# Performance work log

Hardware: AMD Instinct MI355X
Metric: run time of the kernel (lower is better)

The kernel has to match this reference:

```python
import jax, jax.numpy as jnp
import numpy as np
from jax import lax

BETA = 0.95
THRESHOLD = 1.0
B, T, D_IN, D_OUT = 128, 512, 512, 512


def setup_inputs() -> dict:
    key = jax.random.key(0)
    k1, k2, k3 = jax.random.split(key, 3)
    x_seq = jax.random.normal(k1, (B, T, D_IN), dtype=jnp.float32)
    W = jax.random.normal(k2, (D_OUT, D_IN), dtype=jnp.float32) * (1.0 / np.sqrt(D_IN))
    b = jax.random.normal(k3, (D_OUT,), dtype=jnp.float32) * 0.01
    return {"x_seq": x_seq, "W": W, "b": b}


def reference(x_seq, W, b):
    # Batch the linear across all timesteps: [B,T,D_in] @ [D_out,D_in]^T -> [B,T,D_out]
    currents = jnp.einsum('bti,oi->bto', x_seq, W) + b

    def step(mem, cur):  # mem: [B, D_out], cur: [B, D_out]
        mem = BETA * mem + cur
        spk = (mem > THRESHOLD).astype(mem.dtype)
        return mem - spk * THRESHOLD, spk

    mem0 = jnp.zeros((x_seq.shape[0], W.shape[0]), dtype=x_seq.dtype)
    _, spikes_tbd = lax.scan(step, mem0, jnp.swapaxes(currents, 0, 1))  # [T,B,D]
    spikes = jnp.swapaxes(spikes_tbd, 0, 1)  # [B,T,D]
    return spikes, spikes.sum()
```

## Files before the change

kernel.cpp:

```cpp
#include <hip/hip_runtime.h>
#include <hip/hip_bf16.h>

#define M_TOT 65536
#define K_DIM 512
#define N_DIM 512
#define T_STEPS 512
#define BETA 0.95f

#define BM 128
#define BN 128
#define BK 64

typedef __attribute__((ext_vector_type(8))) short bf16x8;
typedef __attribute__((ext_vector_type(8))) unsigned short u16x8;
typedef __attribute__((ext_vector_type(4))) float f32x4;

#define X_ELEMS ((size_t)M_TOT * K_DIM)
#define W_ELEMS ((size_t)N_DIM * K_DIM)
#define WS_NEEDED ((X_ELEMS + W_ELEMS + X_ELEMS) * 2)

static __device__ __forceinline__ unsigned short f2bf(float f) {
    __hip_bfloat16 h = __float2bfloat16(f);
    return __builtin_bit_cast(unsigned short, h);
}
static __device__ __forceinline__ float bf2f(unsigned short u) {
    return __builtin_bit_cast(float, (unsigned int)u << 16);
}

__global__ __launch_bounds__(256) void convert_bf16(
    const float* __restrict__ X, const float* __restrict__ W,
    unsigned short* __restrict__ Xb, unsigned short* __restrict__ Wb,
    float* __restrict__ sum_out)
{
    const size_t gid = (size_t)blockIdx.x * 256 + threadIdx.x;
    if (gid == 0) *sum_out = 0.0f;
    const size_t NXT = X_ELEMS / 8;
    if (gid < NXT) {
        const float4 v0 = *(const float4*)(X + gid * 8);
        const float4 v1 = *(const float4*)(X + gid * 8 + 4);
        u16x8 o;
        o[0] = f2bf(v0.x); o[1] = f2bf(v0.y); o[2] = f2bf(v0.z); o[3] = f2bf(v0.w);
        o[4] = f2bf(v1.x); o[5] = f2bf(v1.y); o[6] = f2bf(v1.z); o[7] = f2bf(v1.w);
        *(u16x8*)(Xb + gid * 8) = o;
    } else {
        const size_t g2 = gid - NXT;
        const float4 v0 = *(const float4*)(W + g2 * 8);
        const float4 v1 = *(const float4*)(W + g2 * 8 + 4);
        u16x8 o;
        o[0] = f2bf(v0.x); o[1] = f2bf(v0.y); o[2] = f2bf(v0.z); o[3] = f2bf(v0.w);
        o[4] = f2bf(v1.x); o[5] = f2bf(v1.y); o[6] = f2bf(v1.z); o[7] = f2bf(v1.w);
        *(u16x8*)(Wb + g2 * 8) = o;
    }
}

__global__ __launch_bounds__(256) void gemm_fast(
    const unsigned short* __restrict__ Xb,
    const unsigned short* __restrict__ Wb,
    const float* __restrict__ bias,
    unsigned short* __restrict__ Cb)
{
    __shared__ alignas(16) unsigned short Xs[2][BM][BK];
    __shared__ alignas(16) unsigned short Ws[2][BN][BK];

    const int lin  = blockIdx.x;
    const int swz  = (lin & 7) * 256 + (lin >> 3);
    const int mtile = swz >> 2;
    const int ntile = swz & 3;

    const int tid  = threadIdx.x;
    const int lane = tid & 63;
    const int wave = tid >> 6;
    const int wr = wave >> 1;
    const int wc = wave & 1;

    const int row0 = mtile * BM;
    const int col0 = ntile * BN;

    f32x4 acc[4][4] = {};

    const int srow = lane >> 3;
    const int scb  = (lane & 7) ^ (srow & 7);
    const unsigned short* xsrc[4];
    const unsigned short* wsrc[4];
    #pragma unroll
    for (int j = 0; j < 4; ++j) {
        const int ra = row0 + wave * 32 + j * 8 + srow;
        const int rb = col0 + wave * 32 + j * 8 + srow;
        xsrc[j] = Xb + (size_t)ra * K_DIM + scb * 8;
        wsrc[j] = Wb + (size_t)rb * K_DIM + scb * 8;
    }

    const int frow = lane & 15;
    const int cblk = lane >> 4;

    #pragma unroll
    for (int j = 0; j < 4; ++j) {
        __builtin_amdgcn_global_load_lds(
            (const __attribute__((address_space(1))) unsigned int*)(const void*)(xsrc[j]),
            (__attribute__((address_space(3))) unsigned int*)(void*)(&Xs[0][wave * 32 + j * 8][0]),
            16, 0, 0);
        __builtin_amdgcn_global_load_lds(
            (const __attribute__((address_space(1))) unsigned int*)(const void*)(wsrc[j]),
            (__attribute__((address_space(3))) unsigned int*)(void*)(&Ws[0][wave * 32 + j * 8][0]),
            16, 0, 0);
    }

    #pragma unroll
    for (int t = 0; t < 8; ++t) {
        const int cur = t & 1;
        __syncthreads();

        if (t < 7) {
            #pragma unroll
            for (int j = 0; j < 4; ++j) {
                __builtin_amdgcn_global_load_lds(
                    (const __attribute__((address_space(1))) unsigned int*)(const void*)(xsrc[j] + (t + 1) * BK),
                    (__attribute__((address_space(3))) unsigned int*)(void*)(&Xs[cur ^ 1][wave * 32 + j * 8][0]),
                    16, 0, 0);
                __builtin_amdgcn_global_load_lds(
                    (const __attribute__((address_space(1))) unsigned int*)(const void*)(wsrc[j] + (t + 1) * BK),
                    (__attribute__((address_space(3))) unsigned int*)(void*)(&Ws[cur ^ 1][wave * 32 + j * 8][0]),
                    16, 0, 0);
            }
        }

        #pragma unroll
        for (int kh = 0; kh < 2; ++kh) {
            bf16x8 afr[4], bfr[4];
            #pragma unroll
            for (int m = 0; m < 4; ++m) {
                int row = wr * 64 + m * 16 + frow;
                int c = (kh * 4 + cblk) ^ (row & 7);
                afr[m] = *(const bf16x8*)(&Xs[cur][row][c * 8]);
            }
            #pragma unroll
            for (int n = 0; n < 4; ++n) {
                int row = wc * 64 + n * 16 + frow;
                int c = (kh * 4 + cblk) ^ (row & 7);
                bfr[n] = *(const bf16x8*)(&Ws[cur][row][c * 8]);
            }
            #pragma unroll
            for (int m = 0; m < 4; ++m)
                #pragma unroll
                for (int n = 0; n < 4; ++n)
                    acc[m][n] = __builtin_amdgcn_mfma_f32_16x16x32_bf16(
                        afr[m], bfr[n], acc[m][n], 0, 0, 0);
        }
    }

    const int crow_base = (lane >> 4) * 4;
    const int ccol = lane & 15;
    #pragma unroll
    for (int n = 0; n < 4; ++n) {
        int col = col0 + wc * 64 + n * 16 + ccol;
        float bv = bias[col];
        #pragma unroll
        for (int m = 0; m < 4; ++m) {
            int rowb = row0 + wr * 64 + m * 16 + crow_base;
            #pragma unroll
            for (int r = 0; r < 4; ++r) {
                Cb[(size_t)(rowb + r) * N_DIM + col] = f2bf(acc[m][n][r] + bv);
            }
        }
    }
}

__global__ __launch_bounds__(256) void lif_scan(
    const unsigned short* __restrict__ Cb,
    float* __restrict__ S,
    float* __restrict__ sum_out)
{
    const int idx = blockIdx.x * 256 + threadIdx.x;
    const size_t base = (size_t)(idx >> 9) * (T_STEPS * N_DIM) + (idx & 511);
    const unsigned short* p = Cb + base;
    float* q = S + base;

    float mem = 0.0f;
    int count = 0;
    float a[32], b[32];

    #pragma unroll
    for (int j = 0; j < 32; ++j)
        a[j] = bf2f(p[(size_t)j * N_DIM]);

    for (int t = 0; t < T_STEPS; t += 64) {
        #pragma unroll
        for (int j = 0; j < 32; ++j)
            b[j] = bf2f(p[(size_t)(t + 32 + j) * N_DIM]);
        #pragma unroll
        for (int j = 0; j < 32; ++j) {
            mem = BETA * mem + a[j];
            float spk = (mem > 1.0f) ? 1.0f : 0.0f;
            mem -= spk;
            __builtin_nontemporal_store(spk, q + (size_t)(t + j) * N_DIM);
            count += (int)spk;
        }
        if (t + 64 < T_STEPS) {
            #pragma unroll
            for (int j = 0; j < 32; ++j)
                a[j] = bf2f(p[(size_t)(t + 64 + j) * N_DIM]);
        }
        #pragma unroll
        for (int j = 0; j < 32; ++j) {
            mem = BETA * mem + b[j];
            float spk = (mem > 1.0f) ? 1.0f : 0.0f;
            mem -= spk;
            __builtin_nontemporal_store(spk, q + (size_t)(t + 32 + j) * N_DIM);
            count += (int)spk;
        }
    }

    #pragma unroll
    for (int off = 32; off > 0; off >>= 1)
        count += __shfl_down(count, off);
    __shared__ int wsum[4];
    if ((threadIdx.x & 63) == 0) wsum[threadIdx.x >> 6] = count;
    __syncthreads();
    if (threadIdx.x == 0) {
        int tot = wsum[0] + wsum[1] + wsum[2] + wsum[3];
        atomicAdd(sum_out, (float)tot);
    }
}

static __device__ __forceinline__ void stage_tiles(
    unsigned short (*__restrict__ Xs)[BK], unsigned short (*__restrict__ Ws)[BK],
    const float4* xr, const float4* wv, int sr0, int skg)
{
    #pragma unroll
    for (int i = 0; i < 8; ++i) {
        int r   = sr0 + i * 16;
        int kgs = skg ^ ((r & 7) << 3);
        ushort4 xb, wb;
        xb.x = f2bf(xr[i].x); xb.y = f2bf(xr[i].y); xb.z = f2bf(xr[i].z); xb.w = f2bf(xr[i].w);
        wb.x = f2bf(wv[i].x); wb.y = f2bf(wv[i].y); wb.z = f2bf(wv[i].z); wb.w = f2bf(wv[i].w);
        *(ushort4*)(&Xs[r][kgs]) = xb;
        *(ushort4*)(&Ws[r][kgs]) = wb;
    }
}

__global__ __launch_bounds__(256, 2) void gemm_slow(
    const float* __restrict__ X, const float* __restrict__ W,
    const float* __restrict__ bias, float* __restrict__ C,
    float* __restrict__ sum_out)
{
    __shared__ unsigned short Xs[2][BM][BK];
    __shared__ unsigned short Ws[2][BN][BK];

    const int lin  = blockIdx.x;
    const int swz  = (lin & 7) * 256 + (lin >> 3);
    const int mtile = swz >> 2;
    const int ntile = swz & 3;

    const int tid  = threadIdx.x;
    const int lane = tid & 63;
    const int wave = tid >> 6;
    const int wr = wave >> 1;
    const int wc = wave & 1;

    if (lin == 0 && tid == 0) *sum_out = 0.0f;

    const int row0 = mtile * BM;
    const int col0 = ntile * BN;

    f32x4 acc[4][4] = {};

    const int sr0 = tid >> 4;
    const int skg = (tid & 15) << 2;
    const float* xbase = X + (size_t)row0 * K_DIM + skg;
    const float* wbase = W + (size_t)col0 * K_DIM + skg;

    float4 xr[8], wv[8];
    #pragma unroll
    for (int i = 0; i < 8; ++i) {
        int r = sr0 + i * 16;
        xr[i] = *(const float4*)(xbase + (size_t)r * K_DIM);
        wv[i] = *(const float4*)(wbase + (size_t)r * K_DIM);
    }
    stage_tiles(Xs[0], Ws[0], xr, wv, sr0, skg);

    const int frow = lane & 15;
    const int cblk = lane >> 4;

    for (int t = 0; t < 8; ++t) {
        __syncthreads();
        if (t < 7) {
            const int k0n = (t + 1) * BK;
            #pragma unroll
            for (int i = 0; i < 8; ++i) {
                int r = sr0 + i * 16;
                xr[i] = *(const float4*)(xbase + (size_t)r * K_DIM + k0n);
                wv[i] = *(const float4*)(wbase + (size_t)r * K_DIM + k0n);
            }
        }
        unsigned short (*Xbuf)[BK] = Xs[t & 1];
        unsigned short (*Wbuf)[BK] = Ws[t & 1];
        #pragma unroll
        for (int kh = 0; kh < 2; ++kh) {
            bf16x8 afr[4], bfr[4];
            #pragma unroll
            for (int m = 0; m < 4; ++m) {
                int row = wr * 64 + m * 16 + frow;
                int c = (kh * 4 + cblk) ^ (row & 7);
                afr[m] = *(const bf16x8*)(&Xbuf[row][c * 8]);
            }
            #pragma unroll
            for (int n = 0; n < 4; ++n) {
                int row = wc * 64 + n * 16 + frow;
                int c = (kh * 4 + cblk) ^ (row & 7);
                bfr[n] = *(const bf16x8*)(&Wbuf[row][c * 8]);
            }
            #pragma unroll
            for (int m = 0; m < 4; ++m)
                #pragma unroll
                for (int n = 0; n < 4; ++n)
                    acc[m][n] = __builtin_amdgcn_mfma_f32_16x16x32_bf16(
                        afr[m], bfr[n], acc[m][n], 0, 0, 0);
        }
        if (t < 7)
            stage_tiles(Xs[(t + 1) & 1], Ws[(t + 1) & 1], xr, wv, sr0, skg);
    }

    const int crow_base = (lane >> 4) * 4;
    const int ccol = lane & 15;
    #pragma unroll
    for (int n = 0; n < 4; ++n) {
        int col = col0 + wc * 64 + n * 16 + ccol;
        float bv = bias[col];
        #pragma unroll
        for (int m = 0; m < 4; ++m) {
            int rowb = row0 + wr * 64 + m * 16 + crow_base;
            #pragma unroll
            for (int r = 0; r < 4; ++r) {
                C[(size_t)(rowb + r) * N_DIM + col] = acc[m][n][r] + bv;
            }
        }
    }
}

__global__ __launch_bounds__(256) void lif_scan_f32(
    float* __restrict__ C, float* __restrict__ sum_out)
{
    const int idx = blockIdx.x * 256 + threadIdx.x;
    float* p = C + (size_t)(idx >> 9) * (T_STEPS * N_DIM) + (idx & 511);
    float mem = 0.0f;
    int count = 0;
    for (int t = 0; t < T_STEPS; t += 8) {
        float cur[8];
        #pragma unroll
        for (int j = 0; j < 8; ++j) cur[j] = p[(size_t)(t + j) * N_DIM];
        #pragma unroll
        for (int j = 0; j < 8; ++j) {
            mem = BETA * mem + cur[j];
            float spk = (mem > 1.0f) ? 1.0f : 0.0f;
            mem -= spk;
            p[(size_t)(t + j) * N_DIM] = spk;
            count += (int)spk;
        }
    }
    #pragma unroll
    for (int off = 32; off > 0; off >>= 1) count += __shfl_down(count, off);
    __shared__ int wsum[4];
    if ((threadIdx.x & 63) == 0) wsum[threadIdx.x >> 6] = count;
    __syncthreads();
    if (threadIdx.x == 0)
        atomicAdd(sum_out, (float)(wsum[0] + wsum[1] + wsum[2] + wsum[3]));
}

extern "C" void kernel_launch(void* const* d_in, const int* in_sizes, int n_in,
                              void* d_out, int out_size, void* d_ws, size_t ws_size,
                              hipStream_t stream) {
    const float* X    = (const float*)d_in[0];
    const float* W    = (const float*)d_in[1];
    const float* bias = (const float*)d_in[2];
    float* out = (float*)d_out;
    float* sum_slot = out + (size_t)M_TOT * N_DIM;

    if (ws_size >= WS_NEEDED) {
        unsigned short* Xb = (unsigned short*)d_ws;
        unsigned short* Wb = Xb + X_ELEMS;
        unsigned short* Cb = Wb + W_ELEMS;
        const int nconv = (int)((X_ELEMS / 8 + W_ELEMS / 8) / 256);
        convert_bf16<<<nconv, 256, 0, stream>>>(X, W, Xb, Wb, sum_slot);
        gemm_fast<<<(M_TOT / BM) * (N_DIM / BN), 256, 0, stream>>>(Xb, Wb, bias, Cb);
        lif_scan<<<M_TOT / 256, 256, 0, stream>>>(Cb, out, sum_slot);
    } else {
        gemm_slow<<<(M_TOT / BM) * (N_DIM / BN), 256, 0, stream>>>(X, W, bias, out, sum_slot);
        lif_scan_f32<<<M_TOT / 256, 256, 0, stream>>>(out, sum_slot);
    }
}
```

Baseline: 317.2 us.

## Fuse GEMM and LIF scan into one kernel, keeping currents in LDS

Replaces the separate bf16 GEMM and LIF scan kernels with one fused kernel. Each block owns one batch element and a 128-wide output slice, and loops over four 128-timestep tiles. After each tile's GEMM it writes the currents into swizzled LDS, and 128 threads run the recurrence serially over those timesteps. This removes the round trip of the intermediate current tensor through HBM and one kernel launch. In exchange the grid shrinks to 512 blocks, and half the threads idle during a serial scan that blocks the next GEMM tile, which can cost MFMA utilisation and occupancy.

```diff
diff --git a/kernel.cpp b/kernel.cpp
--- a/kernel.cpp
+++ b/kernel.cpp
@@ -17,7 +17,7 @@
 
 #define X_ELEMS ((size_t)M_TOT * K_DIM)
 #define W_ELEMS ((size_t)N_DIM * K_DIM)
-#define WS_NEEDED ((X_ELEMS + W_ELEMS + X_ELEMS) * 2)
+#define WS_NEEDED ((X_ELEMS + W_ELEMS) * 2)
 
 static __device__ __forceinline__ unsigned short f2bf(float f) {
     __hip_bfloat16 h = __float2bfloat16(f);
@@ -26,6 +26,10 @@
 static __device__ __forceinline__ float bf2f(unsigned short u) {
     return __builtin_bit_cast(float, (unsigned int)u << 16);
 }
+
+#define GLL(src, dst) __builtin_amdgcn_global_load_lds( \
+    (const __attribute__((address_space(1))) unsigned int*)(const void*)(src), \
+    (__attribute__((address_space(3))) unsigned int*)(void*)(dst), 16, 0, 0)
 
 __global__ __launch_bounds__(256) void convert_bf16(
     const float* __restrict__ X, const float* __restrict__ W,
@@ -53,19 +57,20 @@
     }
 }
 
-__global__ __launch_bounds__(256) void gemm_fast(
+__global__ __launch_bounds__(256) void fused_gemm_lif(
     const unsigned short* __restrict__ Xb,
     const unsigned short* __restrict__ Wb,
     const float* __restrict__ bias,
-    unsigned short* __restrict__ Cb)
-{
-    __shared__ alignas(16) unsigned short Xs[2][BM][BK];
-    __shared__ alignas(16) unsigned short Ws[2][BN][BK];
-
-    const int lin  = blockIdx.x;
-    const int swz  = (lin & 7) * 256 + (lin >> 3);
-    const int mtile = swz >> 2;
-    const int ntile = swz & 3;
+    float* __restrict__ S,
+    float* __restrict__ sum_out)
+{
+    __shared__ alignas(16) unsigned short lds[32768];
+    __shared__ int wsum[4];
+
+    const int lin = blockIdx.x;
+    const int swz = (lin & 7) * 64 + (lin >> 3);
+    const int b   = swz >> 2;
+    const int d0  = (swz & 3) * 128;
 
     const int tid  = threadIdx.x;
     const int lane = tid & 63;
@@ -73,153 +78,124 @@
     const int wr = wave >> 1;
     const int wc = wave & 1;
 
-    const int row0 = mtile * BM;
-    const int col0 = ntile * BN;
-
-    f32x4 acc[4][4] = {};
-
     const int srow = lane >> 3;
     const int scb  = (lane & 7) ^ (srow & 7);
-    const unsigned short* xsrc[4];
+
     const unsigned short* wsrc[4];
     #pragma unroll
-    for (int j = 0; j < 4; ++j) {
-        const int ra = row0 + wave * 32 + j * 8 + srow;
-        const int rb = col0 + wave * 32 + j * 8 + srow;
-        xsrc[j] = Xb + (size_t)ra * K_DIM + scb * 8;
-        wsrc[j] = Wb + (size_t)rb * K_DIM + scb * 8;
-    }
+    for (int j = 0; j < 4; ++j)
+        wsrc[j] = Wb + (size_t)(d0 + wave * 32 + j * 8 + srow) * K_DIM + scb * 8;
 
     const int frow = lane & 15;
     const int cblk = lane >> 4;
 
-    #pragma unroll
-    for (int j = 0; j < 4; ++j) {
-        __builtin_amdgcn_global_load_lds(
-            (const __attribute__((address_space(1))) unsigned int*)(const void*)(xsrc[j]),
-            (__attribute__((address_space(3))) unsigned int*)(void*)(&Xs[0][wave * 32 + j * 8][0]),
-            16, 0, 0);
-        __builtin_amdgcn_global_load_lds(
-            (const __attribute__((address_space(1))) unsigned int*)(const void*)(wsrc[j]),
-            (__attribute__((address_space(3))) unsigned int*)(void*)(&Ws[0][wave * 32 + j * 8][0]),
-            16, 0, 0);
-    }
-
-    #pragma unroll
-    for (int t = 0; t < 8; ++t) {
-        const int cur = t & 1;
-        __syncthreads();
-
-        if (t < 7) {
-            #pragma unroll
-            for (int j = 0; j < 4; ++j) {
-                __builtin_amdgcn_global_load_lds(
-                    (const __attribute__((address_space(1))) unsigned int*)(const void*)(xsrc[j] + (t + 1) * BK),
-                    (__attribute__((address_space(3))) unsigned int*)(void*)(&Xs[cur ^ 1][wave * 32 + j * 8][0]),
-                    16, 0, 0);
-                __builtin_amdgcn_global_load_lds(
-                    (const __attribute__((address_space(1))) unsigned int*)(const void*)(wsrc[j] + (t + 1) * BK),
-                    (__attribute__((address_space(3))) unsigned int*)(void*)(&Ws[cur ^ 1][wave * 32 + j * 8][0]),
-                    16, 0, 0);
-            }
-        }
-
-        #pragma unroll
-        for (int kh = 0; kh < 2; ++kh) {
-            bf16x8 afr[4], bfr[4];
-            #pragma unroll
-            for (int m = 0; m < 4; ++m) {
-                int row = wr * 64 + m * 16 + frow;
-                int c = (kh * 4 + cblk) ^ (row & 7);
-                afr[m] = *(const bf16x8*)(&Xs[cur][row][c * 8]);
-            }
-            #pragma unroll
-            for (int n = 0; n < 4; ++n) {
-                int row = wc * 64 + n * 16 + frow;
-                int c = (kh * 4 + cblk) ^ (row & 7);
-                bfr[n] = *(const bf16x8*)(&Ws[cur][row][c * 8]);
-            }
-            #pragma unroll
-            for (int m = 0; m < 4; ++m)
-                #pragma unroll
-                for (int n = 0; n < 4; ++n)
-                    acc[m][n] = __builtin_amdgcn_mfma_f32_16x16x32_bf16(
-                        afr[m], bfr[n], acc[m][n], 0, 0, 0);
-        }
-    }
-
-    const int crow_base = (lane >> 4) * 4;
-    const int ccol = lane & 15;
-    #pragma unroll
-    for (int n = 0; n < 4; ++n) {
-        int col = col0 + wc * 64 + n * 16 + ccol;
-        float bv = bias[col];
-        #pragma unroll
-        for (int m = 0; m < 4; ++m) {
-            int rowb = row0 + wr * 64 + m * 16 + crow_base;
-            #pragma unroll
-            for (int r = 0; r < 4; ++r) {
-                Cb[(size_t)(rowb + r) * N_DIM + col] = f2bf(acc[m][n][r] + bv);
-            }
-        }
-    }
-}
-
-__global__ __launch_bounds__(256) void lif_scan(
-    const unsigned short* __restrict__ Cb,
-    float* __restrict__ S,
-    float* __restrict__ sum_out)
-{
-    const int idx = blockIdx.x * 256 + threadIdx.x;
-    const size_t base = (size_t)(idx >> 9) * (T_STEPS * N_DIM) + (idx & 511);
-    const unsigned short* p = Cb + base;
-    float* q = S + base;
+    float bv[4];
+    #pragma unroll
+    for (int n = 0; n < 4; ++n)
+        bv[n] = bias[d0 + wc * 64 + n * 16 + frow];
 
     float mem = 0.0f;
     int count = 0;
-    float a[32], b[32];
-
-    #pragma unroll
-    for (int j = 0; j < 32; ++j)
-        a[j] = bf2f(p[(size_t)j * N_DIM]);
-
-    for (int t = 0; t < T_STEPS; t += 64) {
-        #pragma unroll
-        for (int j = 0; j < 32; ++j)
-            b[j] = bf2f(p[(size_t)(t + 32 + j) * N_DIM]);
-        #pragma unroll
-        for (int j = 0; j < 32; ++j) {
-            mem = BETA * mem + a[j];
-            float spk = (mem > 1.0f) ? 1.0f : 0.0f;
-            mem -= spk;
-            __builtin_nontemporal_store(spk, q + (size_t)(t + j) * N_DIM);
-            count += (int)spk;
-        }
-        if (t + 64 < T_STEPS) {
-            #pragma unroll
-            for (int j = 0; j < 32; ++j)
-                a[j] = bf2f(p[(size_t)(t + 64 + j) * N_DIM]);
-        }
-        #pragma unroll
-        for (int j = 0; j < 32; ++j) {
-            mem = BETA * mem + b[j];
-            float spk = (mem > 1.0f) ? 1.0f : 0.0f;
-            mem -= spk;
-            __builtin_nontemporal_store(spk, q + (size_t)(t + 32 + j) * N_DIM);
-            count += (int)spk;
+
+    for (int mt = 0; mt < 4; ++mt) {
+        const int row0 = b * T_STEPS + mt * 128;
+        const unsigned short* xsrc[4];
+        #pragma unroll
+        for (int j = 0; j < 4; ++j)
+            xsrc[j] = Xb + (size_t)(row0 + wave * 32 + j * 8 + srow) * K_DIM + scb * 8;
+
+        #pragma unroll
+        for (int j = 0; j < 4; ++j) {
+            GLL(xsrc[j], &lds[(wave * 32 + j * 8) * BK]);
+            GLL(wsrc[j], &lds[8192 + (wave * 32 + j * 8) * BK]);
+        }
+
+        f32x4 acc[4][4] = {};
+
+        #pragma unroll
+        for (int k = 0; k < 8; ++k) {
+            const int cur = k & 1;
+            __syncthreads();
+            if (k < 7) {
+                const int nb = (cur ^ 1) * 16384;
+                #pragma unroll
+                for (int j = 0; j < 4; ++j) {
+                    GLL(xsrc[j] + (k + 1) * BK, &lds[nb + (wave * 32 + j * 8) * BK]);
+                    GLL(wsrc[j] + (k + 1) * BK, &lds[nb + 8192 + (wave * 32 + j * 8) * BK]);
+                }
+            }
+            const int cb = cur * 16384;
+            #pragma unroll
+            for (int kh = 0; kh < 2; ++kh) {
+                bf16x8 afr[4], bfr[4];
+                #pragma unroll
+                for (int m = 0; m < 4; ++m) {
+                    int row = wr * 64 + m * 16 + frow;
+                    int c = (kh * 4 + cblk) ^ (row & 7);
+                    afr[m] = *(const bf16x8*)(&lds[cb + row * BK + c * 8]);
+                }
+                #pragma unroll
+                for (int n = 0; n < 4; ++n) {
+                    int row = wc * 64 + n * 16 + frow;
+                    int c = (kh * 4 + cblk) ^ (row & 7);
+                    bfr[n] = *(const bf16x8*)(&lds[cb + 8192 + row * BK + c * 8]);
+                }
+                #pragma unroll
+                for (int m = 0; m < 4; ++m)
+                    #pragma unroll
+                    for (int n = 0; n < 4; ++n)
+                        acc[m][n] = __builtin_amdgcn_mfma_f32_16x16x32_bf16(
+                            afr[m], bfr[n], acc[m][n], 0, 0, 0);
+            }
+        }
+
+        __syncthreads();
+
+        #pragma unroll
+        for (int n = 0; n < 4; ++n) {
+            const int d_ = wc * 64 + n * 16 + frow;
+            #pragma unroll
+            for (int m = 0; m < 4; ++m) {
+                const int tb = wr * 64 + m * 16 + ((lane >> 4) << 2);
+                #pragma unroll
+                for (int r = 0; r < 4; ++r) {
+                    const int t_ = tb + r;
+                    lds[16384 + t_ * 128 + (d_ ^ (((t_ >> 2) & 3) << 4))] =
+                        f2bf(acc[m][n][r] + bv[n]);
+                }
+            }
+        }
+
+        __syncthreads();
+
+        if (tid < 128) {
+            float* qb = S + (size_t)row0 * N_DIM + d0 + tid;
+            for (int t2 = 0; t2 < 128; t2 += 8) {
+                float v[8];
+                #pragma unroll
+                for (int j = 0; j < 8; ++j) {
+                    const int tt = t2 + j;
+                    v[j] = bf2f(lds[16384 + tt * 128 + (tid ^ (((tt >> 2) & 3) << 4))]);
+                }
+                #pragma unroll
+                for (int j = 0; j < 8; ++j) {
+                    mem = BETA * mem + v[j];
+                    float spk = (mem > 1.0f) ? 1.0f : 0.0f;
+                    mem -= spk;
+                    __builtin_nontemporal_store(spk, qb + (size_t)(t2 + j) * N_DIM);
+                    count += (int)spk;
+                }
+            }
         }
     }
 
     #pragma unroll
     for (int off = 32; off > 0; off >>= 1)
         count += __shfl_down(count, off);
-    __shared__ int wsum[4];
-    if ((threadIdx.x & 63) == 0) wsum[threadIdx.x >> 6] = count;
+    if ((tid & 63) == 0) wsum[tid >> 6] = count;
     __syncthreads();
-    if (threadIdx.x == 0) {
-        int tot = wsum[0] + wsum[1] + wsum[2] + wsum[3];
-        atomicAdd(sum_out, (float)tot);
-    }
+    if (tid == 0)
+        atomicAdd(sum_out, (float)(wsum[0] + wsum[1] + wsum[2] + wsum[3]));
 }
 
 static __device__ __forceinline__ void stage_tiles(
@@ -325,13 +301,13 @@
     #pragma unroll
     for (int n = 0; n < 4; ++n) {
         int col = col0 + wc * 64 + n * 16 + ccol;
-        float bv = bias[col];
+        float bvv = bias[col];
         #pragma unroll
         for (int m = 0; m < 4; ++m) {
             int rowb = row0 + wr * 64 + m * 16 + crow_base;
             #pragma unroll
             for (int r = 0; r < 4; ++r) {
-                C[(size_t)(rowb + r) * N_DIM + col] = acc[m][n][r] + bv;
+                C[(size_t)(rowb + r) * N_DIM + col] = acc[m][n][r] + bvv;
             }
         }
     }
@@ -378,11 +354,9 @@
     if (ws_size >= WS_NEEDED) {
         unsigned short* Xb = (unsigned short*)d_ws;
         unsigned short* Wb = Xb + X_ELEMS;
-        unsigned short* Cb = Wb + W_ELEMS;
         const int nconv = (int)((X_ELEMS / 8 + W_ELEMS / 8) / 256);
         convert_bf16<<<nconv, 256, 0, stream>>>(X, W, Xb, Wb, sum_slot);
-        gemm_fast<<<(M_TOT / BM) * (N_DIM / BN), 256, 0, stream>>>(Xb, Wb, bias, Cb);
-        lif_scan<<<M_TOT / 256, 256, 0, stream>>>(Cb, out, sum_slot);
+        fused_gemm_lif<<<512, 256, 0, stream>>>(Xb, Wb, bias, out, sum_slot);
     } else {
         gemm_slow<<<(M_TOT / BM) * (N_DIM / BN), 256, 0, stream>>>(X, W, bias, out, sum_slot);
         lif_scan_f32<<<M_TOT / 256, 256, 0, stream>>>(out, sum_slot);
```

After: 274.7 us. -13.4%, faster.
